# Kernel tuning notes

Hardware: AMD Instinct MI355X
Metric: run time of the kernel (lower is better)

Reference implementation:

```python
import jax, jax.numpy as jnp
import numpy as np

S, B, DIM = 1024, 4, 768
N_EXPERTS = 8
# hidden_dim = 256 * ceil(int(2*4*dim/3)/256) = 2048 for dim=768
HID = 2048


def setup_inputs() -> dict:
    key = jax.random.key(0)
    ks = jax.random.split(key, 6)
    scale = 0.02
    return {
        "hidden_states": jax.random.normal(ks[0], (S, B, DIM), dtype=jnp.float32),
        "router_w": jax.random.normal(ks[1], (DIM, N_EXPERTS), dtype=jnp.float32) * scale,
        "router_b": jnp.zeros((N_EXPERTS,), dtype=jnp.float32),
        "w1": jax.random.normal(ks[2], (N_EXPERTS, DIM, HID), dtype=jnp.float32) * scale,
        "w2": jax.random.normal(ks[3], (N_EXPERTS, DIM, HID), dtype=jnp.float32) * scale,
        "w3": jax.random.normal(ks[4], (N_EXPERTS, HID, DIM), dtype=jnp.float32) * scale,
    }


def reference(hidden_states, router_w, router_b, w1, w2, w3):
    s, b, h = hidden_states.shape
    # top-1 router
    route = jax.nn.softmax(hidden_states @ router_w + router_b, axis=2)  # [s,b,E]
    max_prob = jnp.max(route, axis=2).reshape(-1, 1)   # [T,1]
    max_ind = jnp.argmax(route, axis=2).reshape(-1)    # [T]
    x = hidden_states.reshape(-1, h)                   # [T,d]

    out = jnp.zeros_like(x)
    # fixed small loop over experts; masked dispatch (tokens not routed to e
    # are zeroed so they contribute nothing)
    for e in range(N_EXPERTS):
        mask = (max_ind == e)[:, None]                 # [T,1]
        xe = jnp.where(mask, x, 0.0)
        oe = (jax.nn.silu(xe @ w1[e]) * (xe @ w2[e])) @ w3[e]
        out = out + jnp.where(mask, oe, 0.0)

    # original stores expert outputs in a bf16 buffer before the prob combine
    out = out.astype(jnp.bfloat16) * max_prob          # bf16 * f32 -> f32
    return out.reshape(s, b, h)
```

## Files before the change

kernel.cpp:

```cpp
#include <hip/hip_runtime.h>


#define T_TOK 4096
#define DIM   768
#define HID   2048
#define NE    8
#define ECAP  1024

#define KB1 24
#define NB1 128
#define KB2 64
#define NB2 48
#define MBC 64

typedef _Float16 f16x8 __attribute__((ext_vector_type(8)));
typedef float    f32x4 __attribute__((ext_vector_type(4)));

__device__ __forceinline__ float bf16_rne(float v) {
    unsigned u = __float_as_uint(v);
    unsigned r = (u + 0x7fffu + ((u >> 16) & 1u)) & 0xffff0000u;
    return __uint_as_float(r);
}

__device__ __forceinline__ void convert_tile(
    const float* __restrict__ src, _Float16* __restrict__ dst,
    float* Lt, int N, int KBc, int ngrp, int kgrp)
{
    const int t  = threadIdx.x;
    const int c4 = (t & 31) * 4;
    const int r0 = (t >> 5) * 8;
    const float* p = src + (size_t)(kgrp * 64 + r0) * N + ngrp * 128 + c4;
    float4 v[8];
#pragma unroll
    for (int j = 0; j < 8; ++j) v[j] = *(const float4*)(p + (size_t)j * N);
#pragma unroll
    for (int j = 0; j < 8; ++j) {
        float* row = &Lt[(r0 + j) * 130 + c4];
        *(float2*)(row)     = make_float2(v[j].x, v[j].y);
        *(float2*)(row + 2) = make_float2(v[j].z, v[j].w);
    }
    __syncthreads();

    const int l = t & 63, w = t >> 6;
    const int fr = l & 15, fq = l >> 4;
#pragma unroll
    for (int i = 0; i < 4; ++i) {
        const int cell = w * 4 + i;
        const int kbl = cell >> 3, nbl = cell & 7;
        f16x8 h;
#pragma unroll
        for (int j = 0; j < 8; ++j)
            h[j] = (_Float16)Lt[(kbl * 32 + fq * 8 + j) * 130 + nbl * 16 + fr];
        const int nb = ngrp * 8 + nbl, kb = kgrp * 2 + kbl;
        *(f16x8*)(dst + ((size_t)nb * KBc + kb) * 512 + l * 8) = h;
    }
}

__global__ __launch_bounds__(256) void moe_convert_w1_kernel(
    const float* __restrict__ w1, _Float16* __restrict__ w1s)
{
    __shared__ float Lt[64 * 130];
    const int e = blockIdx.x / 192, tile = blockIdx.x % 192;
    convert_tile(w1 + (size_t)e * DIM * HID, w1s + (size_t)e * NB1 * KB1 * 512,
                 Lt, HID, KB1, tile & 15, tile >> 4);
}

__global__ __launch_bounds__(256) void moe_convert_w2_kernel(
    const float* __restrict__ w2, _Float16* __restrict__ w2s)
{
    __shared__ float Lt[64 * 130];
    const int e = blockIdx.x / 192, tile = blockIdx.x % 192;
    convert_tile(w2 + (size_t)e * DIM * HID, w2s + (size_t)e * NB1 * KB1 * 512,
                 Lt, HID, KB1, tile & 15, tile >> 4);
}

__global__ __launch_bounds__(256) void moe_convert_w3_kernel(
    const float* __restrict__ w3, _Float16* __restrict__ w3s)
{
    __shared__ float Lt[64 * 130];
    const int e = blockIdx.x / 192, tile = blockIdx.x % 192;
    convert_tile(w3 + (size_t)e * HID * DIM, w3s + (size_t)e * NB2 * KB2 * 512,
                 Lt, DIM, KB2, tile % 6, tile / 6);
}

__global__ __launch_bounds__(256) void moe_router_kernel(
    const float* __restrict__ X, const float* __restrict__ rw,
    const float* __restrict__ rb, float* __restrict__ probs,
    int* __restrict__ maxind)
{
    const int t = blockIdx.x * 4 + (threadIdx.x >> 6);
    const int l = threadIdx.x & 63;
    const int e = l >> 3;
    const int g = l & 7;
    const float* x = X + (size_t)t * DIM + g * 96;
    const float* w = rw + e;

    double s0 = 0.0, s1 = 0.0;
#pragma unroll
    for (int j4 = 0; j4 < 24; ++j4) {
        const float4 xv = *(const float4*)(x + j4 * 4);
        const int d = (g * 96 + j4 * 4) * NE;
        s0 += (double)xv.x * (double)w[d];
        s1 += (double)xv.y * (double)w[d + NE];
        s0 += (double)xv.z * (double)w[d + 2 * NE];
        s1 += (double)xv.w * (double)w[d + 3 * NE];
    }
    double s = s0 + s1;
    s += __shfl_xor(s, 1, 64);
    s += __shfl_xor(s, 2, 64);
    s += __shfl_xor(s, 4, 64);
    s += (double)rb[e];

    double m = s; int mi = e;
#pragma unroll
    for (int o = 8; o <= 32; o <<= 1) {
        const double om = __shfl_xor(m, o, 64);
        const int   omi = __shfl_xor(mi, o, 64);
        if (om > m || (om == m && omi < mi)) { m = om; mi = omi; }
    }
    float ex = __expf((float)(s - m));
#pragma unroll
    for (int o = 8; o <= 32; o <<= 1) ex += __shfl_xor(ex, o, 64);

    if (l == 0) { probs[t] = 1.0f / ex; maxind[t] = mi; }
}

__global__ __launch_bounds__(256) void moe_lists_kernel(
    const int* __restrict__ maxind, int* __restrict__ counts,
    int* __restrict__ lists)
{
    const int e = blockIdx.x;
    const int tid = threadIdx.x, wid = tid >> 6, lane = tid & 63;
    __shared__ int wsum[4];
    int* dst = lists + e * T_TOK;
    int base = 0;
    for (int t0 = 0; t0 < T_TOK; t0 += 256) {
        const int t = t0 + tid;
        const bool pred = (maxind[t] == e);
        const unsigned long long bal = __ballot(pred);
        const int prefix = __popcll(bal & ((1ull << lane) - 1ull));
        if (lane == 0) wsum[wid] = __popcll(bal);
        __syncthreads();
        int woff = 0;
#pragma unroll
        for (int w2 = 0; w2 < 4; ++w2)
            if (w2 < wid) woff += wsum[w2];
        const int tot = wsum[0] + wsum[1] + wsum[2] + wsum[3];
        if (pred) dst[base + woff + prefix] = t;
        base += tot;
        __syncthreads();
    }
    if (tid == 0) counts[e] = base;
}

__global__ __launch_bounds__(256) void moe_gather_kernel(
    const float* __restrict__ X, const int* __restrict__ lists,
    const int* __restrict__ counts, _Float16* __restrict__ Ag)
{
    const int e = blockIdx.z;
    int cnt = counts[e]; if (cnt > ECAP) cnt = ECAP;
    const int mgrp = blockIdx.y;
    if (mgrp * 64 >= ((cnt + 63) & ~63)) return;
    const int t = threadIdx.x, w = t >> 6, l = t & 63;
    const int mb = mgrp * 4 + w;
    const int m  = mb * 16 + (l & 15);
    const bool valid = (m < cnt);
    const int tok = valid ? lists[e * T_TOK + m] : 0;
    const float* xr = X + (size_t)tok * DIM + (l >> 4) * 8;
#pragma unroll
    for (int i = 0; i < 4; ++i) {
        const int kb = blockIdx.x * 4 + i;
        float4 a = make_float4(0.f, 0.f, 0.f, 0.f), b = a;
        if (valid) {
            a = *(const float4*)(xr + kb * 32);
            b = *(const float4*)(xr + kb * 32 + 4);
        }
        f16x8 h;
        h[0] = (_Float16)a.x; h[1] = (_Float16)a.y; h[2] = (_Float16)a.z; h[3] = (_Float16)a.w;
        h[4] = (_Float16)b.x; h[5] = (_Float16)b.y; h[6] = (_Float16)b.z; h[7] = (_Float16)b.w;
        *(f16x8*)(Ag + ((size_t)(e * MBC + mb) * KB1 + kb) * 512 + l * 8) = h;
    }
}

__global__ __launch_bounds__(256, 3) void moe_gemm1_kernel(
    const _Float16* __restrict__ Ag, const _Float16* __restrict__ w1s,
    const _Float16* __restrict__ w2s, const int* __restrict__ counts,
    _Float16* __restrict__ Hs)
{
    const int e = blockIdx.z;
    int cnt = counts[e]; if (cnt > ECAP) cnt = ECAP;
    const int by = blockIdx.y, bx = blockIdx.x;
    if (by * 128 >= cnt) return;
    const int t = threadIdx.x, w = t >> 6, l = t & 63;
    const int wm = w & 1, wn = w >> 1;

    __shared__ _Float16 Ls[2][16 * 512];

    const int c0s = w * 4;
    const _Float16* gsrc[4];
#pragma unroll
    for (int i = 0; i < 4; ++i) {
        const int c = c0s + i;
        if (c < 8)
            gsrc[i] = Ag  + ((size_t)((e * MBC + by * 8 + c) * KB1)) * 512;
        else if (c < 12)
            gsrc[i] = w1s + ((size_t)((e * NB1 + bx * 4 + (c - 8)) * KB1)) * 512;
        else
            gsrc[i] = w2s + ((size_t)((e * NB1 + bx * 4 + (c - 12)) * KB1)) * 512;
        gsrc[i] += (size_t)l * 8;
    }

    f32x4 acc1[4][2], acc2[4][2];
    const f32x4 zero = {0.f, 0.f, 0.f, 0.f};
#pragma unroll
    for (int i = 0; i < 4; ++i)
#pragma unroll
        for (int j = 0; j < 2; ++j) { acc1[i][j] = zero; acc2[i][j] = zero; }

    f16x8 st0[4], st1[4];
    auto G = [&](f16x8* st, int kb) {
#pragma unroll
        for (int i = 0; i < 4; ++i)
            st[i] = *(const f16x8*)(gsrc[i] + (size_t)kb * 512);
    };
    auto STEP = [&](f16x8* stc, int kb, _Float16* Lb) {
#pragma unroll
        for (int i = 0; i < 4; ++i)
            *(f16x8*)(Lb + (c0s + i) * 512 + l * 8) = stc[i];
        __syncthreads();
        if (kb + 2 < KB1) G(stc, kb + 2);

        f16x8 a[4], p[2], q[2];
#pragma unroll
        for (int i = 0; i < 4; ++i)
            a[i] = *(const f16x8*)(Lb + (wm * 4 + i) * 512 + l * 8);
#pragma unroll
        for (int j = 0; j < 2; ++j) {
            p[j] = *(const f16x8*)(Lb + (8  + wn * 2 + j) * 512 + l * 8);
            q[j] = *(const f16x8*)(Lb + (12 + wn * 2 + j) * 512 + l * 8);
        }
#pragma unroll
        for (int i = 0; i < 4; ++i)
#pragma unroll
            for (int j = 0; j < 2; ++j) {
                acc1[i][j] = __builtin_amdgcn_mfma_f32_16x16x32_f16(a[i], p[j], acc1[i][j], 0, 0, 0);
                acc2[i][j] = __builtin_amdgcn_mfma_f32_16x16x32_f16(a[i], q[j], acc2[i][j], 0, 0, 0);
            }
    };

    G(st0, 0); G(st1, 1);
    for (int kb = 0; kb < KB1; kb += 2) {
        STEP(st0, kb,     &Ls[0][0]);
        STEP(st1, kb + 1, &Ls[1][0]);
    }

    __syncthreads();
    _Float16* Ep = &Ls[0][0] + (size_t)w * (64 * 40);
    const int fq = l >> 4, fr = l & 15;
#pragma unroll
    for (int i = 0; i < 4; ++i)
#pragma unroll
        for (int j = 0; j < 2; ++j)
#pragma unroll
            for (int r = 0; r < 4; ++r) {
                const float h1 = acc1[i][j][r], h2 = acc2[i][j][r];
                const float s  = h1 / (1.f + __expf(-h1)) * h2;
                Ep[(i * 16 + fq * 4 + r) * 40 + j * 16 + fr] = (_Float16)s;
            }
    __syncthreads();
    const int kbH = bx * 2 + wn;
#pragma unroll
    for (int i = 0; i < 4; ++i) {
        f16x8 v = *(const f16x8*)&Ep[(i * 16 + fr) * 40 + fq * 8];
        *(f16x8*)(Hs + ((size_t)((e * MBC + by * 8 + wm * 4 + i) * KB2 + kbH)) * 512 + l * 8) = v;
    }
}

__global__ __launch_bounds__(256, 4) void moe_gemm2_kernel(
    const _Float16* __restrict__ Hs, const _Float16* __restrict__ w3s,
    const int* __restrict__ lists, const int* __restrict__ counts,
    const float* __restrict__ probs, float* __restrict__ out)
{
    const int e = blockIdx.z;
    int cnt = counts[e]; if (cnt > ECAP) cnt = ECAP;
    const int by = blockIdx.y, bx = blockIdx.x;
    if (by * 64 >= cnt) return;
    const int t = threadIdx.x, w = t >> 6, l = t & 63;

    __shared__ _Float16 La[2][8 * 512];

    const _Float16* Asrc = Hs + ((size_t)((e * MBC + by * 4 + w) * KB2)) * 512 + l * 8;
    const int nb0 = e * NB2 + bx * 8 + w * 2;
    const _Float16* Bb = w3s + ((size_t)nb0 * KB2) * 512 + l * 8;

    f32x4 acc[4][2];
    const f32x4 zero = {0.f, 0.f, 0.f, 0.f};
#pragma unroll
    for (int i = 0; i < 4; ++i) { acc[i][0] = zero; acc[i][1] = zero; }

    f16x8 stA[2];
    f16x8 vB0[4], vB1[4];

    auto GA = [&](int s) {
        stA[0] = *(const f16x8*)(Asrc + (size_t)(2 * s)     * 512);
        stA[1] = *(const f16x8*)(Asrc + (size_t)(2 * s + 1) * 512);
    };
    auto GB = [&](f16x8* vB, int s) {
#pragma unroll
        for (int u = 0; u < 2; ++u)
#pragma unroll
            for (int j = 0; j < 2; ++j)
                vB[u * 2 + j] = *(const f16x8*)(Bb + ((size_t)(j * KB2 + 2 * s + u)) * 512);
    };
    auto STEP = [&](int s, const f16x8* curB, f16x8* nxtB, _Float16* Lb) {
        *(f16x8*)(Lb +      w  * 512 + l * 8) = stA[0];
        *(f16x8*)(Lb + (4 + w) * 512 + l * 8) = stA[1];
        __syncthreads();
        if (s + 1 < KB2 / 2) { GA(s + 1); GB(nxtB, s + 1); }
#pragma unroll
        for (int u = 0; u < 2; ++u) {
            f16x8 a[4];
#pragma unroll
            for (int i = 0; i < 4; ++i)
                a[i] = *(const f16x8*)(Lb + (u * 4 + i) * 512 + l * 8);
#pragma unroll
            for (int i = 0; i < 4; ++i)
#pragma unroll
                for (int j = 0; j < 2; ++j)
                    acc[i][j] = __builtin_amdgcn_mfma_f32_16x16x32_f16(a[i], curB[u * 2 + j], acc[i][j], 0, 0, 0);
        }
    };

    GA(0); GB(vB0, 0);
    for (int s2 = 0; s2 < KB2 / 2; s2 += 2) {
        STEP(s2,     vB0, vB1, &La[0][0]);
        STEP(s2 + 1, vB1, vB0, &La[1][0]);
    }

    const int* list = lists + e * T_TOK;
    const int fq = l >> 4, fr = l & 15;
    const int c0 = bx * 128 + w * 32;
#pragma unroll
    for (int i = 0; i < 4; ++i)
#pragma unroll
        for (int r = 0; r < 4; ++r) {
            const int m = by * 64 + i * 16 + fq * 4 + r;
            if (m < cnt) {
                const int tok = list[m];
                const float pb = probs[tok];
                float* orow = out + (size_t)tok * DIM + c0 + fr;
                orow[0]  = bf16_rne(acc[i][0][r]) * pb;
                orow[16] = bf16_rne(acc[i][1][r]) * pb;
            }
        }
}

extern "C" void kernel_launch(void* const* d_in, const int* in_sizes, int n_in,
                              void* d_out, int out_size, void* d_ws, size_t ws_size,
                              hipStream_t stream) {
    const float* X  = (const float*)d_in[0];
    const float* rw = (const float*)d_in[1];
    const float* rb = (const float*)d_in[2];
    const float* w1 = (const float*)d_in[3];
    const float* w2 = (const float*)d_in[4];
    const float* w3 = (const float*)d_in[5];
    float* out = (float*)d_out;

    char* ws = (char*)d_ws;
    int*      counts = (int*)(ws + 0);
    int*      lists  = (int*)(ws + 256);
    float*    probs  = (float*)(ws + 131328);
    const size_t WSZ = 25165824;
    _Float16* w1s = (_Float16*)(ws + 147712);
    _Float16* w2s = (_Float16*)(ws + 147712 + WSZ);
    _Float16* w3s = (_Float16*)(ws + 147712 + 2 * WSZ);
    _Float16* Ag  = (_Float16*)(ws + 147712 + 3 * WSZ);
    _Float16* Hs  = (_Float16*)(ws + 147712 + 3 * WSZ + 12582912);
    int* maxind = (int*)Ag;

    hipLaunchKernelGGL(moe_convert_w1_kernel, dim3(1536), dim3(256), 0, stream, w1, w1s);
    hipLaunchKernelGGL(moe_convert_w2_kernel, dim3(1536), dim3(256), 0, stream, w2, w2s);
    hipLaunchKernelGGL(moe_convert_w3_kernel, dim3(1536), dim3(256), 0, stream, w3, w3s);
    hipLaunchKernelGGL(moe_router_kernel, dim3(T_TOK / 4), dim3(256), 0, stream,
                       X, rw, rb, probs, maxind);
    hipLaunchKernelGGL(moe_lists_kernel, dim3(NE), dim3(256), 0, stream,
                       maxind, counts, lists);
    hipLaunchKernelGGL(moe_gather_kernel, dim3(6, 16, 8), dim3(256), 0, stream,
                       X, lists, counts, Ag);
    hipLaunchKernelGGL(moe_gemm1_kernel, dim3(32, 8, 8), dim3(256), 0, stream,
                       Ag, w1s, w2s, counts, Hs);
    hipLaunchKernelGGL(moe_gemm2_kernel, dim3(6, 16, 8), dim3(256), 0, stream,
                       Hs, w3s, lists, counts, probs, out);
}
```

Baseline: 309.2 us.

## Stage GEMM operand tiles via direct global-to-LDS loads instead of register staging

Both expert GEMM kernels now copy their shared-memory tiles with global_load_lds (buffer-to-LDS DMA) instead of loading into registers and then writing to LDS. The pipeline is restructured into a prefetch-next, compute-current, barrier loop, and gemm1's launch bounds go from 3 to 4 waves per SIMD. This is meant to cut VGPR pressure and the extra LDS write instructions so occupancy can rise. The trade-offs are reliance on barrier ordering of asynchronous LDS writes (vmcnt waits) and possible register spills under the tighter bound.

Measured after the change: 304.5 us. Within noise of the previous version (-1.5%).

```diff
diff --git a/kernel.cpp b/kernel.cpp
--- a/kernel.cpp
+++ b/kernel.cpp
@@ -15,6 +15,14 @@
 
 typedef _Float16 f16x8 __attribute__((ext_vector_type(8)));
 typedef float    f32x4 __attribute__((ext_vector_type(4)));
+
+#define AS1 __attribute__((address_space(1)))
+#define AS3 __attribute__((address_space(3)))
+
+__device__ __forceinline__ void gload_lds16(const _Float16* g, _Float16* l) {
+    __builtin_amdgcn_global_load_lds((const AS1 unsigned int*)g,
+                                     (AS3 unsigned int*)l, 16, 0, 0);
+}
 
 __device__ __forceinline__ float bf16_rne(float v) {
     unsigned u = __float_as_uint(v);
@@ -182,7 +190,7 @@
     }
 }
 
-__global__ __launch_bounds__(256, 3) void moe_gemm1_kernel(
+__global__ __launch_bounds__(256, 4) void moe_gemm1_kernel(
     const _Float16* __restrict__ Ag, const _Float16* __restrict__ w1s,
     const _Float16* __restrict__ w2s, const int* __restrict__ counts,
     _Float16* __restrict__ Hs)
@@ -217,18 +225,17 @@
 #pragma unroll
         for (int j = 0; j < 2; ++j) { acc1[i][j] = zero; acc2[i][j] = zero; }
 
-    f16x8 st0[4], st1[4];
-    auto G = [&](f16x8* st, int kb) {
+    auto STAGE = [&](int kb, _Float16* Lb) {
 #pragma unroll
         for (int i = 0; i < 4; ++i)
-            st[i] = *(const f16x8*)(gsrc[i] + (size_t)kb * 512);
+            gload_lds16(gsrc[i] + (size_t)kb * 512, Lb + (c0s + i) * 512);
     };
-    auto STEP = [&](f16x8* stc, int kb, _Float16* Lb) {
-#pragma unroll
-        for (int i = 0; i < 4; ++i)
-            *(f16x8*)(Lb + (c0s + i) * 512 + l * 8) = stc[i];
-        __syncthreads();
-        if (kb + 2 < KB1) G(stc, kb + 2);
+
+    STAGE(0, &Ls[0][0]);
+    __syncthreads();
+    for (int kb = 0; kb < KB1; ++kb) {
+        _Float16* Lb = &Ls[kb & 1][0];
+        if (kb + 1 < KB1) STAGE(kb + 1, &Ls[(kb + 1) & 1][0]);
 
         f16x8 a[4], p[2], q[2];
 #pragma unroll
@@ -246,15 +253,9 @@
                 acc1[i][j] = __builtin_amdgcn_mfma_f32_16x16x32_f16(a[i], p[j], acc1[i][j], 0, 0, 0);
                 acc2[i][j] = __builtin_amdgcn_mfma_f32_16x16x32_f16(a[i], q[j], acc2[i][j], 0, 0, 0);
             }
-    };
-
-    G(st0, 0); G(st1, 1);
-    for (int kb = 0; kb < KB1; kb += 2) {
-        STEP(st0, kb,     &Ls[0][0]);
-        STEP(st1, kb + 1, &Ls[1][0]);
-    }
-
-    __syncthreads();
+        __syncthreads();
+    }
+
     _Float16* Ep = &Ls[0][0] + (size_t)w * (64 * 40);
     const int fq = l >> 4, fr = l & 15;
 #pragma unroll
@@ -298,12 +299,11 @@
 #pragma unroll
     for (int i = 0; i < 4; ++i) { acc[i][0] = zero; acc[i][1] = zero; }
 
-    f16x8 stA[2];
     f16x8 vB0[4], vB1[4];
 
-    auto GA = [&](int s) {
-        stA[0] = *(const f16x8*)(Asrc + (size_t)(2 * s)     * 512);
-        stA[1] = *(const f16x8*)(Asrc + (size_t)(2 * s + 1) * 512);
+    auto STAGE_A = [&](int s, _Float16* Lb) {
+        gload_lds16(Asrc + (size_t)(2 * s)     * 512, Lb +      w  * 512);
+        gload_lds16(Asrc + (size_t)(2 * s + 1) * 512, Lb + (4 + w) * 512);
     };
     auto GB = [&](f16x8* vB, int s) {
 #pragma unroll
@@ -312,11 +312,9 @@
             for (int j = 0; j < 2; ++j)
                 vB[u * 2 + j] = *(const f16x8*)(Bb + ((size_t)(j * KB2 + 2 * s + u)) * 512);
     };
-    auto STEP = [&](int s, const f16x8* curB, f16x8* nxtB, _Float16* Lb) {
-        *(f16x8*)(Lb +      w  * 512 + l * 8) = stA[0];
-        *(f16x8*)(Lb + (4 + w) * 512 + l * 8) = stA[1];
-        __syncthreads();
-        if (s + 1 < KB2 / 2) { GA(s + 1); GB(nxtB, s + 1); }
+    auto STEP = [&](int s, const f16x8* curB, f16x8* nxtB,
+                    _Float16* Lb, _Float16* Ln) {
+        if (s + 1 < KB2 / 2) { STAGE_A(s + 1, Ln); GB(nxtB, s + 1); }
 #pragma unroll
         for (int u = 0; u < 2; ++u) {
             f16x8 a[4];
@@ -329,12 +327,14 @@
                 for (int j = 0; j < 2; ++j)
                     acc[i][j] = __builtin_amdgcn_mfma_f32_16x16x32_f16(a[i], curB[u * 2 + j], acc[i][j], 0, 0, 0);
         }
+        __syncthreads();
     };
 
-    GA(0); GB(vB0, 0);
+    STAGE_A(0, &La[0][0]); GB(vB0, 0);
+    __syncthreads();
     for (int s2 = 0; s2 < KB2 / 2; s2 += 2) {
-        STEP(s2,     vB0, vB1, &La[0][0]);
-        STEP(s2 + 1, vB1, vB0, &La[1][0]);
+        STEP(s2,     vB0, vB1, &La[0][0], &La[1][0]);
+        STEP(s2 + 1, vB1, vB0, &La[1][0], &La[0][0]);
     }
 
     const int* list = lists + e * T_TOK;
```
